# Performance work log

Measured on AMD Instinct MI355X. Metric: run time of the kernel, lower is better.

The kernel has to match this reference:

```python
import jax, jax.numpy as jnp
import numpy as np
import math

DIM = 768
NUM_HEADS = 12
HEAD_DIM = DIM // NUM_HEADS


def setup_inputs() -> dict:
    key = jax.random.key(0)
    k_x, k_q, k_k, k_v = jax.random.split(key, 4)
    s = 1.0 / math.sqrt(DIM)
    return {
        "x": jax.random.normal(k_x, (2, 2048, DIM), dtype=jnp.float32),
        "Wq": jax.random.normal(k_q, (DIM, DIM), dtype=jnp.float32) * s,
        "Wk": jax.random.normal(k_k, (DIM, DIM), dtype=jnp.float32) * s,
        "Wv": jax.random.normal(k_v, (DIM, DIM), dtype=jnp.float32) * s,
    }


def reference(x, Wq, Wk, Wv):
    b, n, _ = x.shape
    # nn.Linear(dim, dim, bias=False): y = x @ W.T
    def split_heads(y):
        return y.reshape(b, n, NUM_HEADS, HEAD_DIM).transpose(0, 2, 1, 3)  # b h n d
    Q = split_heads(x @ Wq.T)
    K = split_heads(x @ Wk.T)
    V = split_heads(x @ Wv.T)
    scores = jnp.einsum('bhqd,bhkd->bhqk', Q, K)
    # FAITHFUL to source: softmax over the HEADS axis (dim=1), then scale by 1/sqrt(dim)
    attn = jax.nn.softmax(scores, axis=1) / math.sqrt(DIM)
    out = jnp.einsum('bhqk,bhkd->bhqd', attn, V)
    out = out.transpose(0, 2, 1, 3).reshape(b, n, DIM)  # b n (h d)
    return out  # to_out is Identity (project_out=False)
```

## Files before the change

### kernel.cpp

```cpp
#include <hip/hip_runtime.h>

#define DIM 768
#define NHEADS 12
#define HDIM 64
#define BATCH 2
#define SEQ 2048
#define ROWS (BATCH*SEQ)
#define KSPLIT 4

typedef __attribute__((ext_vector_type(8))) _Float16 f16x8;
typedef __attribute__((ext_vector_type(4))) _Float16 f16x4;
typedef __attribute__((ext_vector_type(2))) _Float16 f16x2;
typedef __attribute__((ext_vector_type(4))) float    f32x4;

__device__ __forceinline__ void dma16(const _Float16* g, _Float16* l) {
    __builtin_amdgcn_global_load_lds(
        (const __attribute__((address_space(1))) unsigned int*)g,
        (__attribute__((address_space(3))) unsigned int*)l, 16, 0, 0);
}


__global__ __launch_bounds__(256) void cvt_all(
    const float* __restrict__ x,  const float* __restrict__ wq,
    const float* __restrict__ wk, const float* __restrict__ wv,
    _Float16* __restrict__ xf,  _Float16* __restrict__ wqf,
    _Float16* __restrict__ wkf, _Float16* __restrict__ wvf)
{
    const int lane = threadIdx.x & 63;
    const int wid  = (blockIdx.x * 256 + threadIdx.x) >> 6;
    const float* src; _Float16* dst; int t;
    float sc = 1.0f;
    if (wid < 6144)      { src = x;  dst = xf;  t = wid;        }
    else if (wid < 7296) { src = wq; dst = wqf; t = wid - 6144; sc = 1.4426950408889634f; }
    else if (wid < 8448) { src = wk; dst = wkf; t = wid - 7296; }
    else                 { src = wv; dst = wvf; t = wid - 8448; }
    const int c = lane & 15, quad = lane >> 4;
    const int mt = t / 24, kt = t % 24;
    const float* p = src + (size_t)(mt*16 + c) * 768 + kt*32 + quad*8;
    float4 v0 = *(const float4*)p;
    float4 v1 = *(const float4*)(p + 4);
    f16x8 o;
    o[0]=(_Float16)(v0.x*sc); o[1]=(_Float16)(v0.y*sc); o[2]=(_Float16)(v0.z*sc); o[3]=(_Float16)(v0.w*sc);
    o[4]=(_Float16)(v1.x*sc); o[5]=(_Float16)(v1.y*sc); o[6]=(_Float16)(v1.z*sc); o[7]=(_Float16)(v1.w*sc);
    *reinterpret_cast<f16x8*>(dst + ((size_t)t * 64 + lane) * 8) = o;
}

__global__ __launch_bounds__(512) void gemm3(
    const _Float16* __restrict__ xf, const _Float16* __restrict__ wqkf,
    const _Float16* __restrict__ wvf,
    _Float16* __restrict__ Qf, _Float16* __restrict__ Kf, _Float16* __restrict__ Vkt)
{
    __shared__ _Float16 Ab[2][16*512];
    __shared__ _Float16 Bb[2][8*512];
    const int tid = threadIdx.x, lane = tid & 63, w = tid >> 6;
    const int c = lane & 15, quad = lane >> 4;

    const _Float16 *Af, *Bf;
    int mt0, nt0, mode;
    if ((int)blockIdx.x < 192) {
        int mt = blockIdx.x / 12, nt = blockIdx.x % 12;
        Af = xf; Bf = wqkf; mt0 = mt*16; nt0 = nt*8; mode = 0;
    } else {
        int v = blockIdx.x - 192;
        int mt = v / 32, nt = v % 32;
        Af = wvf; Bf = xf; mt0 = mt*16; nt0 = nt*8; mode = 1;
    }

    auto stage = [&](int kt, int buf) {
#pragma unroll
        for (int u = 0; u < 3; ++u) {
            const int cc = w*3 + u;
            const _Float16* s = (cc < 16) ? Af + ((size_t)(mt0+cc)*24 + kt)*512
                                          : Bf + ((size_t)(nt0+cc-16)*24 + kt)*512;
            _Float16* d = (cc < 16) ? &Ab[buf][cc*512] : &Bb[buf][(cc-16)*512];
            dma16(s + lane*8, d);
        }
    };

    stage(0, 0);
    __syncthreads();

    f32x4 acc[4][4] = {};
    for (int kt = 0; kt < 24; ++kt) {
        const int cur = kt & 1;
        if (kt < 23) stage(kt+1, cur^1);
        f16x8 a[4], b[4];
#pragma unroll
        for (int i = 0; i < 4; ++i)
            a[i] = *(const f16x8*)(&Ab[cur][((w>>1)*4 + i)*512] + lane*8);
#pragma unroll
        for (int j = 0; j < 4; ++j)
            b[j] = *(const f16x8*)(&Bb[cur][((w&1)*4 + j)*512] + lane*8);
#pragma unroll
        for (int i = 0; i < 4; ++i)
#pragma unroll
            for (int j = 0; j < 4; ++j)
                acc[i][j] = __builtin_amdgcn_mfma_f32_16x16x32_f16(a[i], b[j], acc[i][j], 0,0,0);
        __syncthreads();
    }

    _Float16* L = &Ab[0][0] + w*1280;
#pragma unroll
    for (int i2 = 0; i2 < 2; ++i2)
#pragma unroll
        for (int j2 = 0; j2 < 2; ++j2) {
#pragma unroll
            for (int ii = 0; ii < 2; ++ii)
#pragma unroll
                for (int jj = 0; jj < 2; ++jj)
#pragma unroll
                    for (int r = 0; r < 4; ++r)
                        L[(ii*16 + quad*4 + r)*40 + jj*16 + c] =
                            (_Float16)acc[i2*2+ii][j2*2+jj][r];
#pragma unroll
            for (int ii = 0; ii < 2; ++ii) {
                const int mtg = mt0 + (w>>1)*4 + i2*2 + ii;
                if (mode == 0) {
                    f16x8 v = *(const f16x8*)(L + (ii*16 + c)*40 + quad*8);
                    const int nt32 = (nt0 + (w&1)*4)/2 + j2;
                    _Float16* dst = (nt32 < 24)
                        ? Qf + ((size_t)(mtg*24 + nt32)*64 + lane)*8
                        : Kf + ((size_t)(mtg*24 + nt32 - 24)*64 + lane)*8;
                    *(f16x8*)dst = v;
                } else {
#pragma unroll
                    for (int jj = 0; jj < 2; ++jj) {
                        f16x4 v4 = *(const f16x4*)(L + (ii*16 + c)*40 + jj*16 + quad*4);
                        const int kcu = nt0 + (w&1)*4 + j2*2 + jj;
                        *(f16x4*)(Vkt + ((size_t)kcu*48 + mtg)*256 + lane*4) = v4;
                    }
                }
            }
        }
}

__global__ __launch_bounds__(256) __attribute__((amdgpu_waves_per_eu(4)))
void attn_kernel(
    const _Float16* __restrict__ Qf, const _Float16* __restrict__ Kf,
    const _Float16* __restrict__ Vkt,
    float* __restrict__ out,
    _Float16* __restrict__ part)
{
    __shared__ __attribute__((aligned(16))) _Float16 Kb[24*512];
    __shared__ __attribute__((aligned(16))) float    Ps[4][336];
    __shared__ __attribute__((aligned(16))) _Float16 Pl[12][16][20];
    const int tid = threadIdx.x, lane = tid & 63, g = tid >> 6;
    const int c = lane & 15, quad = lane >> 4;

    const int bid = blockIdx.x;
    const int rb = (bid & 7)*128 + (bid >> 3);
    const int qb = rb & 127;
    const int ks = (rb >> 7) & 3;
    const int b  = rb >> 9;
    const int qt16  = b*128 + qb;
    const int qrow0 = qt16*16;
    const int kb16  = b*128 + ks*32;
    const int psoff = quad*84 + c*4;

    f16x8 qreg[6];
#pragma unroll
    for (int u = 0; u < 6; ++u)
        qreg[u] = *(const f16x8*)(Qf + ((size_t)(qt16*24 + g*6 + u)*64 + lane)*8);

    const _Float16* Vb0 = Vkt + ((size_t)kb16*48 + g)*256 + lane*4;

#pragma unroll
    for (int u = 0; u < 6; ++u)
        dma16(Kf + ((size_t)kb16*24 + g*6 + u)*512 + lane*8, &Kb[(g*6+u)*512]);
    __syncthreads();

    f32x4 o_acc[12] = {};
    f16x4 vv[12];
    f32x4 e3[3];

    for (int t = 0; t < 32; ++t) {
#pragma unroll
        for (int hh = 0; hh < 3; ++hh) {
            f16x8 ka = *(const f16x8*)(&Kb[(g*6 + hh*2    )*512] + lane*8);
            f16x8 k2 = *(const f16x8*)(&Kb[(g*6 + hh*2 + 1)*512] + lane*8);
            f32x4 a = {};
            a = __builtin_amdgcn_mfma_f32_16x16x32_f16(ka, qreg[hh*2],   a, 0,0,0);
            a = __builtin_amdgcn_mfma_f32_16x16x32_f16(k2, qreg[hh*2+1], a, 0,0,0);
            f32x4 ee;
#pragma unroll
            for (int r = 0; r < 4; ++r) ee[r] = __builtin_amdgcn_exp2f(a[r]);
            e3[hh] = ee;
        }
        {
            f32x4 ps;
#pragma unroll
            for (int r = 0; r < 4; ++r) ps[r] = e3[0][r] + e3[1][r] + e3[2][r];
            *(f32x4*)&Ps[g][psoff] = ps;
        }
        if (t > 0) {
#pragma unroll
            for (int h = 0; h < 12; ++h) {
                f16x4 pf = *(const f16x4*)&Pl[h][c][quad*4];
                o_acc[h] = __builtin_amdgcn_mfma_f32_16x16x16f16(vv[h], pf, o_acc[h], 0,0,0);
            }
        }
        __syncthreads();
        if (t < 31) {
#pragma unroll
            for (int u = 0; u < 6; ++u)
                dma16(Kf + ((size_t)(kb16+t+1)*24 + g*6 + u)*512 + lane*8,
                      &Kb[(g*6+u)*512]);
        }
        {
            f32x4 s0 = *(const f32x4*)&Ps[0][psoff];
            f32x4 s1 = *(const f32x4*)&Ps[1][psoff];
            f32x4 s2 = *(const f32x4*)&Ps[2][psoff];
            f32x4 s3 = *(const f32x4*)&Ps[3][psoff];
            f32x4 inv;
#pragma unroll
            for (int r = 0; r < 4; ++r)
                inv[r] = __builtin_amdgcn_rcpf(
                    (s0[r]+s1[r]+s2[r]+s3[r]) * 27.712812921102035f);
#pragma unroll
            for (int hh = 0; hh < 3; ++hh) {
                f16x4 pw;
#pragma unroll
                for (int r = 0; r < 4; ++r) pw[r] = (_Float16)(e3[hh][r]*inv[r]);
                *(f16x4*)&Pl[g*3+hh][c][quad*4] = pw;
            }
        }
#pragma unroll
        for (int h = 0; h < 12; ++h)
            vv[h] = *(const f16x4*)(Vb0 + ((size_t)t*48 + h*4)*256);
        __syncthreads();
    }
#pragma unroll
    for (int h = 0; h < 12; ++h) {
        f16x4 pf = *(const f16x4*)&Pl[h][c][quad*4];
        o_acc[h] = __builtin_amdgcn_mfma_f32_16x16x16f16(vv[h], pf, o_acc[h], 0,0,0);
    }

    if (ks == 0) {
#pragma unroll
        for (int h = 0; h < 12; ++h)
            *(f32x4*)(out + (size_t)(qrow0 + c)*DIM + h*64 + g*16 + quad*4)
                = o_acc[h];
    } else {
        _Float16* dst = part + (size_t)(ks - 1) * ROWS * DIM;
#pragma unroll
        for (int h = 0; h < 12; ++h) {
            f16x4 v;
#pragma unroll
            for (int r = 0; r < 4; ++r) v[r] = (_Float16)o_acc[h][r];
            *(f16x4*)(dst + (size_t)(qrow0 + c)*DIM + h*64 + g*16 + quad*4) = v;
        }
    }
}

__global__ __launch_bounds__(256) void reduce_add4(
    float* __restrict__ out, const _Float16* __restrict__ part, int n4)
{
    int i = blockIdx.x * 256 + threadIdx.x;
    if (i >= n4) return;
    float4 o = reinterpret_cast<float4*>(out)[i];
    const size_t N = (size_t)ROWS * DIM;
#pragma unroll
    for (int p = 0; p < 3; ++p) {
        f16x4 v = reinterpret_cast<const f16x4*>(part + p * N)[i];
        o.x += (float)v[0]; o.y += (float)v[1]; o.z += (float)v[2]; o.w += (float)v[3];
    }
    reinterpret_cast<float4*>(out)[i] = o;
}

extern "C" void kernel_launch(void* const* d_in, const int* in_sizes, int n_in,
                              void* d_out, int out_size, void* d_ws, size_t ws_size,
                              hipStream_t stream)
{
    const float* x  = (const float*)d_in[0];
    const float* Wq = (const float*)d_in[1];
    const float* Wk = (const float*)d_in[2];
    const float* Wv = (const float*)d_in[3];

    _Float16* ws  = (_Float16*)d_ws;
    const size_t XS = (size_t)ROWS * DIM;
    const size_t WS = (size_t)DIM * DIM;
    _Float16* xf   = ws;
    _Float16* wqf  = xf  + XS;
    _Float16* wkf  = wqf + WS;
    _Float16* wvf  = wkf + WS;
    _Float16* Qf   = wvf + WS;
    _Float16* Kf   = Qf  + XS;
    _Float16* Vkt  = Kf  + XS;
    _Float16* part = Vkt + XS;

    cvt_all<<<2400, 256, 0, stream>>>(x, Wq, Wk, Wv, xf, wqf, wkf, wvf);
    gemm3<<<288, 512, 0, stream>>>(xf, wqf, wvf, Qf, Kf, Vkt);
    attn_kernel<<<BATCH * KSPLIT * 128, 256, 0, stream>>>(
        Qf, Kf, Vkt, (float*)d_out, part);
    reduce_add4<<<(int)(XS/4 + 255)/256, 256, 0, stream>>>(
        (float*)d_out, part, (int)(XS/4));
}
```

Before: 187.1 us.

## Split attention into log-denominator pass and per-head recompute pass, drop K-split reduce

Replaces the fused K-split attention kernel and its partial-sum reduction with two kernels. The first computes, for every query-key 16x16 tile, the log of the sum over heads of exp(scores), with the 1/sqrt(dim) scale folded in, and stores it to a float buffer. The second runs one wave per (query tile, head) over all keys, recomputes the scores, and subtracts the stored log before exponentiating to get normalized probabilities for the PV MMA. This removes the LDS cross-head exchange, the barriers and the fp16 partial-output reduction. In exchange QK^T is computed twice, and a 2048x2048x2-sized float buffer must be written and then read back, with K and V loaded straight from global memory instead of through LDS.

```diff
diff --git a/kernel.cpp b/kernel.cpp
--- a/kernel.cpp
+++ b/kernel.cpp
@@ -6,11 +6,9 @@
 #define BATCH 2
 #define SEQ 2048
 #define ROWS (BATCH*SEQ)
-#define KSPLIT 4
 
 typedef __attribute__((ext_vector_type(8))) _Float16 f16x8;
 typedef __attribute__((ext_vector_type(4))) _Float16 f16x4;
-typedef __attribute__((ext_vector_type(2))) _Float16 f16x2;
 typedef __attribute__((ext_vector_type(4))) float    f32x4;
 
 __device__ __forceinline__ void dma16(const _Float16* g, _Float16* l) {
@@ -134,137 +132,98 @@
         }
 }
 
-__global__ __launch_bounds__(256) __attribute__((amdgpu_waves_per_eu(4)))
-void attn_kernel(
+__global__ __launch_bounds__(256, 4) void dcalc(
     const _Float16* __restrict__ Qf, const _Float16* __restrict__ Kf,
-    const _Float16* __restrict__ Vkt,
-    float* __restrict__ out,
-    _Float16* __restrict__ part)
-{
-    __shared__ __attribute__((aligned(16))) _Float16 Kb[24*512];
-    __shared__ __attribute__((aligned(16))) float    Ps[4][336];
-    __shared__ __attribute__((aligned(16))) _Float16 Pl[12][16][20];
-    const int tid = threadIdx.x, lane = tid & 63, g = tid >> 6;
+    float* __restrict__ Lc)
+{
+    const int tid = threadIdx.x, lane = tid & 63, w = tid >> 6;
+    const int rb = ((int)blockIdx.x & 7)*128 + ((int)blockIdx.x >> 3);
+    const int u  = rb*4 + w;
+    const int qtl = u & 127;
+    const int kks = (u >> 7) & 15;
+    const int b   = u >> 11;
+    const int qt16 = b*128 + qtl;
+    const int kb16 = b*128 + kks*8;
+
+    f16x8 qreg[24];
+#pragma unroll
+    for (int f = 0; f < 24; ++f)
+        qreg[f] = *(const f16x8*)(Qf + ((size_t)(qt16*24 + f)*64 + lane)*8);
+
+    const _Float16* Kp0 = Kf + ((size_t)kb16*24)*512 + (size_t)lane*8;
+    float* Lp = Lc + ((size_t)(qt16*128 + kks*8))*256 + lane*4;
+
+    for (int i = 0; i < 8; ++i) {
+        const _Float16* Kp = Kp0 + (size_t)i*24*512;
+        f32x4 D = {};
+#pragma unroll
+        for (int h = 0; h < 12; ++h) {
+            f16x8 k0 = *(const f16x8*)(Kp + (2*h    )*512);
+            f16x8 k1 = *(const f16x8*)(Kp + (2*h + 1)*512);
+            f32x4 a = {};
+            a = __builtin_amdgcn_mfma_f32_16x16x32_f16(k0, qreg[2*h    ], a, 0,0,0);
+            a = __builtin_amdgcn_mfma_f32_16x16x32_f16(k1, qreg[2*h + 1], a, 0,0,0);
+#pragma unroll
+            for (int r = 0; r < 4; ++r) D[r] += __builtin_amdgcn_exp2f(a[r]);
+        }
+        f32x4 L;
+#pragma unroll
+        for (int r = 0; r < 4; ++r)
+            L[r] = __log2f(D[r]) + 4.792481250360578f;
+        *(f32x4*)(Lp + (size_t)i*256) = L;
+    }
+}
+
+__global__ __launch_bounds__(256) void attn2(
+    const _Float16* __restrict__ Qf, const _Float16* __restrict__ Kf,
+    const _Float16* __restrict__ Vkt, const float* __restrict__ Lc,
+    float* __restrict__ out)
+{
+    const int tid = threadIdx.x, lane = tid & 63, w = tid >> 6;
     const int c = lane & 15, quad = lane >> 4;
-
-    const int bid = blockIdx.x;
-    const int rb = (bid & 7)*128 + (bid >> 3);
-    const int qb = rb & 127;
-    const int ks = (rb >> 7) & 3;
-    const int b  = rb >> 9;
-    const int qt16  = b*128 + qb;
-    const int qrow0 = qt16*16;
-    const int kb16  = b*128 + ks*32;
-    const int psoff = quad*84 + c*4;
-
-    f16x8 qreg[6];
-#pragma unroll
-    for (int u = 0; u < 6; ++u)
-        qreg[u] = *(const f16x8*)(Qf + ((size_t)(qt16*24 + g*6 + u)*64 + lane)*8);
-
-    const _Float16* Vb0 = Vkt + ((size_t)kb16*48 + g)*256 + lane*4;
-
-#pragma unroll
-    for (int u = 0; u < 6; ++u)
-        dma16(Kf + ((size_t)kb16*24 + g*6 + u)*512 + lane*8, &Kb[(g*6+u)*512]);
-    __syncthreads();
-
-    f32x4 o_acc[12] = {};
-    f16x4 vv[12];
-    f32x4 e3[3];
-
-    for (int t = 0; t < 32; ++t) {
-#pragma unroll
-        for (int hh = 0; hh < 3; ++hh) {
-            f16x8 ka = *(const f16x8*)(&Kb[(g*6 + hh*2    )*512] + lane*8);
-            f16x8 k2 = *(const f16x8*)(&Kb[(g*6 + hh*2 + 1)*512] + lane*8);
-            f32x4 a = {};
-            a = __builtin_amdgcn_mfma_f32_16x16x32_f16(ka, qreg[hh*2],   a, 0,0,0);
-            a = __builtin_amdgcn_mfma_f32_16x16x32_f16(k2, qreg[hh*2+1], a, 0,0,0);
-            f32x4 ee;
-#pragma unroll
-            for (int r = 0; r < 4; ++r) ee[r] = __builtin_amdgcn_exp2f(a[r]);
-            e3[hh] = ee;
-        }
-        {
-            f32x4 ps;
-#pragma unroll
-            for (int r = 0; r < 4; ++r) ps[r] = e3[0][r] + e3[1][r] + e3[2][r];
-            *(f32x4*)&Ps[g][psoff] = ps;
-        }
-        if (t > 0) {
-#pragma unroll
-            for (int h = 0; h < 12; ++h) {
-                f16x4 pf = *(const f16x4*)&Pl[h][c][quad*4];
-                o_acc[h] = __builtin_amdgcn_mfma_f32_16x16x16f16(vv[h], pf, o_acc[h], 0,0,0);
-            }
-        }
-        __syncthreads();
-        if (t < 31) {
-#pragma unroll
-            for (int u = 0; u < 6; ++u)
-                dma16(Kf + ((size_t)(kb16+t+1)*24 + g*6 + u)*512 + lane*8,
-                      &Kb[(g*6+u)*512]);
-        }
-        {
-            f32x4 s0 = *(const f32x4*)&Ps[0][psoff];
-            f32x4 s1 = *(const f32x4*)&Ps[1][psoff];
-            f32x4 s2 = *(const f32x4*)&Ps[2][psoff];
-            f32x4 s3 = *(const f32x4*)&Ps[3][psoff];
-            f32x4 inv;
-#pragma unroll
-            for (int r = 0; r < 4; ++r)
-                inv[r] = __builtin_amdgcn_rcpf(
-                    (s0[r]+s1[r]+s2[r]+s3[r]) * 27.712812921102035f);
-#pragma unroll
-            for (int hh = 0; hh < 3; ++hh) {
-                f16x4 pw;
-#pragma unroll
-                for (int r = 0; r < 4; ++r) pw[r] = (_Float16)(e3[hh][r]*inv[r]);
-                *(f16x4*)&Pl[g*3+hh][c][quad*4] = pw;
-            }
-        }
-#pragma unroll
-        for (int h = 0; h < 12; ++h)
-            vv[h] = *(const f16x4*)(Vb0 + ((size_t)t*48 + h*4)*256);
-        __syncthreads();
-    }
-#pragma unroll
-    for (int h = 0; h < 12; ++h) {
-        f16x4 pf = *(const f16x4*)&Pl[h][c][quad*4];
-        o_acc[h] = __builtin_amdgcn_mfma_f32_16x16x16f16(vv[h], pf, o_acc[h], 0,0,0);
-    }
-
-    if (ks == 0) {
-#pragma unroll
-        for (int h = 0; h < 12; ++h)
-            *(f32x4*)(out + (size_t)(qrow0 + c)*DIM + h*64 + g*16 + quad*4)
-                = o_acc[h];
-    } else {
-        _Float16* dst = part + (size_t)(ks - 1) * ROWS * DIM;
-#pragma unroll
-        for (int h = 0; h < 12; ++h) {
-            f16x4 v;
-#pragma unroll
-            for (int r = 0; r < 4; ++r) v[r] = (_Float16)o_acc[h][r];
-            *(f16x4*)(dst + (size_t)(qrow0 + c)*DIM + h*64 + g*16 + quad*4) = v;
-        }
-    }
-}
-
-__global__ __launch_bounds__(256) void reduce_add4(
-    float* __restrict__ out, const _Float16* __restrict__ part, int n4)
-{
-    int i = blockIdx.x * 256 + threadIdx.x;
-    if (i >= n4) return;
-    float4 o = reinterpret_cast<float4*>(out)[i];
-    const size_t N = (size_t)ROWS * DIM;
-#pragma unroll
-    for (int p = 0; p < 3; ++p) {
-        f16x4 v = reinterpret_cast<const f16x4*>(part + p * N)[i];
-        o.x += (float)v[0]; o.y += (float)v[1]; o.z += (float)v[2]; o.w += (float)v[3];
-    }
-    reinterpret_cast<float4*>(out)[i] = o;
+    const int rb = ((int)blockIdx.x & 7)*96 + ((int)blockIdx.x >> 3);
+    const int u  = rb*4 + w;
+    const int qtl = u & 127;
+    const int v  = u >> 7;
+    const int h  = v % 12;
+    const int b  = v / 12;
+    const int qt16 = b*128 + qtl;
+    const int kb16 = b*128;
+
+    f16x8 q0 = *(const f16x8*)(Qf + ((size_t)(qt16*24 + 2*h    )*64 + lane)*8);
+    f16x8 q1 = *(const f16x8*)(Qf + ((size_t)(qt16*24 + 2*h + 1)*64 + lane)*8);
+
+    const _Float16* Kp0 = Kf  + ((size_t)(kb16*24 + 2*h))*512 + (size_t)lane*8;
+    const _Float16* Vp0 = Vkt + ((size_t)(kb16*48 + h*4))*256 + (size_t)lane*4;
+    const float*    Lp0 = Lc  + ((size_t)qt16*128)*256 + lane*4;
+
+    f32x4 o_acc[4] = {};
+
+#pragma unroll 2
+    for (int t = 0; t < 128; ++t) {
+        const _Float16* Kp = Kp0 + (size_t)t*24*512;
+        f16x8 k0 = *(const f16x8*)(Kp);
+        f16x8 k1 = *(const f16x8*)(Kp + 512);
+        f32x4 Lt = *(const f32x4*)(Lp0 + (size_t)t*256);
+        f32x4 a = {};
+        a = __builtin_amdgcn_mfma_f32_16x16x32_f16(k0, q0, a, 0,0,0);
+        a = __builtin_amdgcn_mfma_f32_16x16x32_f16(k1, q1, a, 0,0,0);
+        f16x4 pp;
+#pragma unroll
+        for (int r = 0; r < 4; ++r)
+            pp[r] = (_Float16)__builtin_amdgcn_exp2f(a[r] - Lt[r]);
+        const _Float16* Vp = Vp0 + (size_t)t*48*256;
+#pragma unroll
+        for (int dt = 0; dt < 4; ++dt) {
+            f16x4 vt = *(const f16x4*)(Vp + dt*256);
+            o_acc[dt] = __builtin_amdgcn_mfma_f32_16x16x16f16(vt, pp, o_acc[dt], 0,0,0);
+        }
+    }
+
+    float* op = out + (size_t)(qt16*16 + c)*DIM + h*64 + quad*4;
+#pragma unroll
+    for (int dt = 0; dt < 4; ++dt)
+        *(f32x4*)(op + dt*16) = o_acc[dt];
 }
 
 extern "C" void kernel_launch(void* const* d_in, const int* in_sizes, int n_in,
@@ -286,12 +245,10 @@
     _Float16* Qf   = wvf + WS;
     _Float16* Kf   = Qf  + XS;
     _Float16* Vkt  = Kf  + XS;
-    _Float16* part = Vkt + XS;
+    float*    Lc   = (float*)(Vkt + XS);
 
     cvt_all<<<2400, 256, 0, stream>>>(x, Wq, Wk, Wv, xf, wqf, wkf, wvf);
     gemm3<<<288, 512, 0, stream>>>(xf, wqf, wvf, Qf, Kf, Vkt);
-    attn_kernel<<<BATCH * KSPLIT * 128, 256, 0, stream>>>(
-        Qf, Kf, Vkt, (float*)d_out, part);
-    reduce_add4<<<(int)(XS/4 + 255)/256, 256, 0, stream>>>(
-        (float*)d_out, part, (int)(XS/4));
-}
+    dcalc<<<1024, 256, 0, stream>>>(Qf, Kf, Lc);
+    attn2<<<768, 256, 0, stream>>>(Qf, Kf, Vkt, Lc, (float*)d_out);
+}
```

New measurement: 218.7 us. +16.9%, slower.
